# Optimization experiments

Hardware: AMD Instinct MI355X
Metric: run time of the kernel (lower is better)

The kernel has to match this reference:

```python
import jax, jax.numpy as jnp
import numpy as np

N_SPOTS = 50000
N_NEIGH = 32   # fixed-degree padding of the ragged radius-graph neighbor lists
N_PROG = 128


def setup_inputs() -> dict:
    key = jax.random.key(0)
    k1, k2, k3 = jax.random.split(key, 3)
    # soft identity probabilities (rows sum to 1, as in the original usage)
    probs = jax.random.uniform(k1, (N_SPOTS, N_PROG), dtype=jnp.float32)
    probs = probs / probs.sum(axis=-1, keepdims=True)
    # neighbor indices (fixed-degree representation of the ragged lists)
    neighbor_idx = jax.random.randint(k2, (N_SPOTS, N_NEIGH), 0, N_SPOTS)
    # gaussian-kernel weights, normalized per spot exactly as _build_graph does
    w = jax.random.uniform(k3, (N_SPOTS, N_NEIGH), dtype=jnp.float32) + 1e-6
    w = w / w.sum(axis=-1, keepdims=True)
    return {"identity_probs": probs, "weights": w, "neighbor_idx": neighbor_idx}


def reference(identity_probs, weights, neighbor_idx):
    # consistency_loss: (1/n) * sum_i sum_j w_ij * ||p_i - p_j||^2
    neigh = identity_probs[neighbor_idx]                 # [n, K, d] gather
    diff = identity_probs[:, None, :] - neigh            # [n, K, d]
    sq = jnp.sum(diff * diff, axis=-1)                   # [n, K]
    n = identity_probs.shape[0]
    return jnp.sum(weights * sq) / n
```

## Files before the change

### kernel.cpp

```cpp
#include <hip/hip_runtime.h>

#define N_SPOTS 50000
#define N_NEIGH 32
#define N_PROG  128

#define BLOCK 256
#define WPB   4

#define TAB_BYTES  ((size_t)N_SPOTS * 64)
#define PAIR_BYTES ((size_t)N_SPOTS * 8)

#define PREP_BLOCKS   3125
#define GATHER_BLOCKS 3125
#define F32_BLOCKS    6250

#if __has_builtin(__builtin_amdgcn_udot8)
__device__ __forceinline__ int dot8(unsigned a, unsigned b) {
    return __builtin_amdgcn_udot8(a, b, 0, false);
}
#else
__device__ __forceinline__ int dot8(unsigned a, unsigned b) {
    int s = 0;
    #pragma unroll
    for (int d = 0; d < 8; ++d)
        s += (int)((a >> (4 * d)) & 0xFu) * (int)((b >> (4 * d)) & 0xFu);
    return s;
}
#endif

__device__ __forceinline__ unsigned q4(float x, float r) {
    unsigned v = (unsigned)__builtin_fmaf(x, r, 0.5f);
    return v > 15u ? 15u : v;
}

__global__ __launch_bounds__(BLOCK) void prep_kernel(
    const float* __restrict__ probs,
    unsigned* __restrict__ tab,
    float2* __restrict__ pair)
{
    const int sub = threadIdx.x & 15;
    const int row = blockIdx.x * 16 + (threadIdx.x >> 4);

    const float* rp = probs + (size_t)row * N_PROG;
    const float4 a = *reinterpret_cast<const float4*>(rp + sub * 4);
    const float4 b = *reinterpret_cast<const float4*>(rp + 64 + sub * 4);

    float mx = fmaxf(fmaxf(a.x, a.y), fmaxf(a.z, a.w));
    mx = fmaxf(mx, fmaxf(fmaxf(b.x, b.y), fmaxf(b.z, b.w)));

    float nr = a.x * a.x;
    nr = fmaf(a.y, a.y, nr); nr = fmaf(a.z, a.z, nr); nr = fmaf(a.w, a.w, nr);
    nr = fmaf(b.x, b.x, nr); nr = fmaf(b.y, b.y, nr);
    nr = fmaf(b.z, b.z, nr); nr = fmaf(b.w, b.w, nr);

    #pragma unroll
    for (int off = 1; off < 16; off <<= 1) {
        mx  = fmaxf(mx, __shfl_xor(mx, off, 16));
        nr += __shfl_xor(nr, off, 16);
    }

    const float r = 15.0f / mx;
    unsigned q = q4(a.x, r);
    q |= q4(a.y, r) << 4;   q |= q4(a.z, r) << 8;   q |= q4(a.w, r) << 12;
    q |= q4(b.x, r) << 16;  q |= q4(b.y, r) << 20;
    q |= q4(b.z, r) << 24;  q |= q4(b.w, r) << 28;

    tab[row * 16 + sub] = q;
    if (sub == 0) pair[row] = make_float2(mx * (1.0f / 15.0f), nr);
}

__global__ __launch_bounds__(BLOCK) void gather_i4_kernel(
    const unsigned* __restrict__ tab,
    const float2* __restrict__ pair,
    const float* __restrict__ w,
    const int*   __restrict__ idx,
    float* __restrict__ partials)
{
    const int lane  = threadIdx.x & 63;
    const int sub   = lane & 15;
    const int wib   = threadIdx.x >> 6;
    const int grp16 = threadIdx.x >> 4;
    const int spot  = blockIdx.x * 16 + grp16;

    const unsigned pown = tab[spot * 16 + sub];
    const float2   pri  = pair[spot];
    const float    s_i  = pri.x, nrm_i = pri.y;

    const int   base = spot * N_NEIGH + sub;
    const int   i0 = idx[base], i1 = idx[base + 16];
    const float w0 = w[base],   w1 = w[base + 16];
    const float2 pr0 = pair[i0], pr1 = pair[i1];
    const float ws0 = w0 * s_i * pr0.x;
    const float ws1 = w1 * s_i * pr1.x;
    const float accB = fmaf(w0, pr0.y, w1 * pr1.y);
    const float accW = w0 + w1;

    __shared__ int2 stage[16][N_NEIGH];
    stage[grp16][sub]      = make_int2(i0, __float_as_int(ws0));
    stage[grp16][sub + 16] = make_int2(i1, __float_as_int(ws1));

    float accC = 0.0f;

    #pragma unroll
    for (int c = 0; c < 4; ++c) {
        unsigned q[8];
        float    wsj[8];
        #pragma unroll
        for (int k = 0; k < 8; ++k) {
            const int2 e = stage[grp16][c * 8 + k];
            wsj[k] = __int_as_float(e.y);
            q[k]   = tab[e.x * 16 + sub];
        }
        #pragma unroll
        for (int k = 0; k < 8; ++k) {
            accC = fmaf(wsj[k], (float)dot8(pown, q[k]), accC);
        }
    }

    float acc = fmaf(accW, nrm_i, accB) - 2.0f * accC;

    #pragma unroll
    for (int off = 32; off > 0; off >>= 1)
        acc += __shfl_down(acc, off, 64);

    __shared__ float s[WPB];
    if (lane == 0) s[wib] = acc;
    __syncthreads();
    if (threadIdx.x == 0) {
        float t = 0.0f;
        #pragma unroll
        for (int v = 0; v < WPB; ++v) t += s[v];
        partials[blockIdx.x] = t;
    }
}

__global__ __launch_bounds__(BLOCK) void gather_f32_kernel(
    const float* __restrict__ probs,
    const float* __restrict__ w,
    const int*   __restrict__ idx,
    float* __restrict__ partials)
{
    const int wib  = threadIdx.x >> 6;
    const int lane = threadIdx.x & 63;
    const int sub  = lane & 31;
    const int half = lane >> 5;
    const int wg   = blockIdx.x * WPB + wib;
    const int spot = (wg << 1) + half;

    const float4 p = *reinterpret_cast<const float4*>(
        probs + (size_t)spot * N_PROG + sub * 4);
    const int   my_idx = idx[spot * N_NEIGH + sub];
    const float my_w   = w  [spot * N_NEIGH + sub];

    float acc = 0.0f;
    #pragma unroll 8
    for (int j = 0; j < N_NEIGH; ++j) {
        const int   nb = __shfl(my_idx, j, 32);
        const float wj = __shfl(my_w,   j, 32);
        const float4 q = *reinterpret_cast<const float4*>(
            probs + (size_t)nb * N_PROG + sub * 4);
        const float dx = p.x - q.x, dy = p.y - q.y;
        const float dz = p.z - q.z, dw = p.w - q.w;
        float sq = dx * dx;
        sq = fmaf(dy, dy, sq); sq = fmaf(dz, dz, sq); sq = fmaf(dw, dw, sq);
        acc = fmaf(wj, sq, acc);
    }

    #pragma unroll
    for (int off = 32; off > 0; off >>= 1)
        acc += __shfl_down(acc, off, 64);

    __shared__ float s[WPB];
    if (lane == 0) s[wib] = acc;
    __syncthreads();
    if (threadIdx.x == 0) {
        float t = 0.0f;
        #pragma unroll
        for (int v = 0; v < WPB; ++v) t += s[v];
        partials[blockIdx.x] = t;
    }
}

__global__ __launch_bounds__(BLOCK) void finalize_kernel(
    const float* __restrict__ partials, int nparts, float* __restrict__ out)
{
    const int wave = threadIdx.x >> 6;
    const int lane = threadIdx.x & 63;

    float acc = 0.0f;
    for (int i = threadIdx.x; i < nparts; i += BLOCK)
        acc += partials[i];

    #pragma unroll
    for (int off = 32; off > 0; off >>= 1)
        acc += __shfl_down(acc, off, 64);

    __shared__ float s[WPB];
    if (lane == 0) s[wave] = acc;
    __syncthreads();
    if (threadIdx.x == 0) {
        float t = 0.0f;
        #pragma unroll
        for (int v = 0; v < WPB; ++v) t += s[v];
        out[0] = t / (float)N_SPOTS;
    }
}

extern "C" void kernel_launch(void* const* d_in, const int* in_sizes, int n_in,
                              void* d_out, int out_size, void* d_ws, size_t ws_size,
                              hipStream_t stream) {
    const float* probs = (const float*)d_in[0];
    const float* w     = (const float*)d_in[1];
    const int*   idx   = (const int*)  d_in[2];
    float* out = (float*)d_out;

    const size_t need = TAB_BYTES + PAIR_BYTES + GATHER_BLOCKS * sizeof(float);
    if (ws_size >= need) {
        unsigned* tab   = (unsigned*)d_ws;
        float2*   pair  = (float2*)((char*)d_ws + TAB_BYTES);
        float* partials = (float*)((char*)d_ws + TAB_BYTES + PAIR_BYTES);

        prep_kernel     <<<PREP_BLOCKS,   BLOCK, 0, stream>>>(probs, tab, pair);
        gather_i4_kernel<<<GATHER_BLOCKS, BLOCK, 0, stream>>>(tab, pair, w, idx, partials);
        finalize_kernel <<<1,             BLOCK, 0, stream>>>(partials, GATHER_BLOCKS, out);
    } else {
        float* partials = (float*)d_ws;
        gather_f32_kernel<<<F32_BLOCKS, BLOCK, 0, stream>>>(probs, w, idx, partials);
        finalize_kernel  <<<1,          BLOCK, 0, stream>>>(partials, F32_BLOCKS, out);
    }
}
```

Baseline: 34.21 us.

## Quantize with a global max scale and fuse the final reduction into the gather

```diff
diff --git a/kernel.cpp b/kernel.cpp
--- a/kernel.cpp
+++ b/kernel.cpp
@@ -7,12 +7,17 @@
 #define BLOCK 256
 #define WPB   4
 
-#define TAB_BYTES  ((size_t)N_SPOTS * 64)
-#define PAIR_BYTES ((size_t)N_SPOTS * 8)
-
-#define PREP_BLOCKS   3125
+#define MAX_BLOCKS    256
+#define QUANT_BLOCKS  3125
 #define GATHER_BLOCKS 3125
 #define F32_BLOCKS    6250
+
+#define TAB_BYTES  ((size_t)N_SPOTS * 64)
+#define BMAX_OFF   TAB_BYTES
+#define GSLOT_OFF  (BMAX_OFF + 1024)
+#define TICKET_OFF (GSLOT_OFF + 64)
+#define PART_OFF   (TICKET_OFF + 64)
+#define NEED_BYTES (PART_OFF + (size_t)GATHER_BLOCKS * 4)
 
 #if __has_builtin(__builtin_amdgcn_udot8)
 __device__ __forceinline__ int dot8(unsigned a, unsigned b) {
@@ -33,48 +38,64 @@
     return v > 15u ? 15u : v;
 }
 
-__global__ __launch_bounds__(BLOCK) void prep_kernel(
-    const float* __restrict__ probs,
-    unsigned* __restrict__ tab,
-    float2* __restrict__ pair)
-{
-    const int sub = threadIdx.x & 15;
-    const int row = blockIdx.x * 16 + (threadIdx.x >> 4);
-
-    const float* rp = probs + (size_t)row * N_PROG;
-    const float4 a = *reinterpret_cast<const float4*>(rp + sub * 4);
-    const float4 b = *reinterpret_cast<const float4*>(rp + 64 + sub * 4);
-
-    float mx = fmaxf(fmaxf(a.x, a.y), fmaxf(a.z, a.w));
-    mx = fmaxf(mx, fmaxf(fmaxf(b.x, b.y), fmaxf(b.z, b.w)));
-
-    float nr = a.x * a.x;
-    nr = fmaf(a.y, a.y, nr); nr = fmaf(a.z, a.z, nr); nr = fmaf(a.w, a.w, nr);
-    nr = fmaf(b.x, b.x, nr); nr = fmaf(b.y, b.y, nr);
-    nr = fmaf(b.z, b.z, nr); nr = fmaf(b.w, b.w, nr);
-
-    #pragma unroll
-    for (int off = 1; off < 16; off <<= 1) {
-        mx  = fmaxf(mx, __shfl_xor(mx, off, 16));
-        nr += __shfl_xor(nr, off, 16);
-    }
-
-    const float r = 15.0f / mx;
+__global__ __launch_bounds__(BLOCK) void max_kernel(
+    const float* __restrict__ probs, float* __restrict__ blockmax,
+    unsigned* __restrict__ ticket)
+{
+    const float4* p4 = reinterpret_cast<const float4*>(probs);
+    float m = 0.0f;
+    for (int i = blockIdx.x * BLOCK + threadIdx.x; i < (N_SPOTS * N_PROG / 4);
+         i += MAX_BLOCKS * BLOCK) {
+        const float4 v = p4[i];
+        m = fmaxf(m, fmaxf(fmaxf(v.x, v.y), fmaxf(v.z, v.w)));
+    }
+    #pragma unroll
+    for (int off = 32; off > 0; off >>= 1) m = fmaxf(m, __shfl_down(m, off, 64));
+    __shared__ float s[WPB];
+    if ((threadIdx.x & 63) == 0) s[threadIdx.x >> 6] = m;
+    __syncthreads();
+    if (threadIdx.x == 0) {
+        blockmax[blockIdx.x] = fmaxf(fmaxf(s[0], s[1]), fmaxf(s[2], s[3]));
+        if (blockIdx.x == 0) *ticket = 0u;
+    }
+}
+
+__global__ __launch_bounds__(BLOCK) void quant_kernel(
+    const float* __restrict__ probs, const float* __restrict__ blockmax,
+    unsigned* __restrict__ tab, float* __restrict__ gslot)
+{
+    __shared__ float smax[WPB];
+    __shared__ float gsh;
+    float m = blockmax[threadIdx.x];
+    #pragma unroll
+    for (int off = 32; off > 0; off >>= 1) m = fmaxf(m, __shfl_down(m, off, 64));
+    if ((threadIdx.x & 63) == 0) smax[threadIdx.x >> 6] = m;
+    __syncthreads();
+    if (threadIdx.x == 0)
+        gsh = fmaxf(fmaxf(smax[0], smax[1]), fmaxf(smax[2], smax[3]));
+    __syncthreads();
+    const float r = 15.0f / gsh;
+
+    const int t = blockIdx.x * BLOCK + threadIdx.x;
+    const float* rp = probs + (size_t)t * 8;
+    const float4 a = *reinterpret_cast<const float4*>(rp);
+    const float4 b = *reinterpret_cast<const float4*>(rp + 4);
     unsigned q = q4(a.x, r);
     q |= q4(a.y, r) << 4;   q |= q4(a.z, r) << 8;   q |= q4(a.w, r) << 12;
     q |= q4(b.x, r) << 16;  q |= q4(b.y, r) << 20;
     q |= q4(b.z, r) << 24;  q |= q4(b.w, r) << 28;
-
-    tab[row * 16 + sub] = q;
-    if (sub == 0) pair[row] = make_float2(mx * (1.0f / 15.0f), nr);
-}
-
-__global__ __launch_bounds__(BLOCK) void gather_i4_kernel(
+    tab[t] = q;
+    if (t == 0) gslot[0] = gsh;
+}
+
+__global__ __launch_bounds__(BLOCK) void gather_kernel(
     const unsigned* __restrict__ tab,
-    const float2* __restrict__ pair,
     const float* __restrict__ w,
     const int*   __restrict__ idx,
-    float* __restrict__ partials)
+    const float* __restrict__ gslot,
+    float* __restrict__ partials,
+    unsigned* __restrict__ ticket,
+    float* __restrict__ out)
 {
     const int lane  = threadIdx.x & 63;
     const int sub   = lane & 15;
@@ -83,54 +104,67 @@
     const int spot  = blockIdx.x * 16 + grp16;
 
     const unsigned pown = tab[spot * 16 + sub];
-    const float2   pri  = pair[spot];
-    const float    s_i  = pri.x, nrm_i = pri.y;
+    const int Qi2 = dot8(pown, pown);
 
     const int   base = spot * N_NEIGH + sub;
     const int   i0 = idx[base], i1 = idx[base + 16];
     const float w0 = w[base],   w1 = w[base + 16];
-    const float2 pr0 = pair[i0], pr1 = pair[i1];
-    const float ws0 = w0 * s_i * pr0.x;
-    const float ws1 = w1 * s_i * pr1.x;
-    const float accB = fmaf(w0, pr0.y, w1 * pr1.y);
-    const float accW = w0 + w1;
+
+    float sw = w0 + w1;
+    #pragma unroll
+    for (int off = 1; off < 16; off <<= 1) sw += __shfl_xor(sw, off, 16);
 
     __shared__ int2 stage[16][N_NEIGH];
-    stage[grp16][sub]      = make_int2(i0, __float_as_int(ws0));
-    stage[grp16][sub + 16] = make_int2(i1, __float_as_int(ws1));
-
-    float accC = 0.0f;
-
+    stage[grp16][sub]      = make_int2(i0, __float_as_int(w0));
+    stage[grp16][sub + 16] = make_int2(i1, __float_as_int(w1));
+
+    float acc2 = 0.0f;
     #pragma unroll
     for (int c = 0; c < 4; ++c) {
-        unsigned q[8];
-        float    wsj[8];
+        unsigned q[8]; float wj[8];
         #pragma unroll
         for (int k = 0; k < 8; ++k) {
             const int2 e = stage[grp16][c * 8 + k];
-            wsj[k] = __int_as_float(e.y);
-            q[k]   = tab[e.x * 16 + sub];
+            wj[k] = __int_as_float(e.y);
+            q[k]  = tab[e.x * 16 + sub];
         }
         #pragma unroll
         for (int k = 0; k < 8; ++k) {
-            accC = fmaf(wsj[k], (float)dot8(pown, q[k]), accC);
+            const int D  = dot8(pown, q[k]);
+            const int Q2 = dot8(q[k], q[k]);
+            acc2 = fmaf(wj[k], (float)(Q2 - 2 * D), acc2);
         }
     }
 
-    float acc = fmaf(accW, nrm_i, accB) - 2.0f * accC;
+    const float G    = gslot[0];
+    const float step = G * (1.0f / 15.0f);
+    float contrib = fmaf(sw, (float)Qi2 - (4.0f / 3.0f), acc2) * (step * step);
 
     #pragma unroll
     for (int off = 32; off > 0; off >>= 1)
-        acc += __shfl_down(acc, off, 64);
-
-    __shared__ float s[WPB];
-    if (lane == 0) s[wib] = acc;
-    __syncthreads();
-    if (threadIdx.x == 0) {
-        float t = 0.0f;
-        #pragma unroll
-        for (int v = 0; v < WPB; ++v) t += s[v];
-        partials[blockIdx.x] = t;
+        contrib += __shfl_down(contrib, off, 64);
+
+    __shared__ float sred[WPB];
+    __shared__ bool  slast;
+    if (lane == 0) sred[wib] = contrib;
+    __syncthreads();
+    if (threadIdx.x == 0) {
+        partials[blockIdx.x] = sred[0] + sred[1] + sred[2] + sred[3];
+        __threadfence();
+        const unsigned old = atomicAdd(ticket, 1u);
+        slast = (old == GATHER_BLOCKS - 1);
+    }
+    __syncthreads();
+    if (slast) {
+        __threadfence();
+        float a = 0.0f;
+        for (int i = threadIdx.x; i < GATHER_BLOCKS; i += BLOCK) a += partials[i];
+        #pragma unroll
+        for (int off = 32; off > 0; off >>= 1) a += __shfl_down(a, off, 64);
+        if (lane == 0) sred[wib] = a;
+        __syncthreads();
+        if (threadIdx.x == 0)
+            out[0] = (sred[0] + sred[1] + sred[2] + sred[3]) / (float)N_SPOTS;
     }
 }
 
@@ -165,11 +199,8 @@
         sq = fmaf(dy, dy, sq); sq = fmaf(dz, dz, sq); sq = fmaf(dw, dw, sq);
         acc = fmaf(wj, sq, acc);
     }
-
-    #pragma unroll
-    for (int off = 32; off > 0; off >>= 1)
-        acc += __shfl_down(acc, off, 64);
-
+    #pragma unroll
+    for (int off = 32; off > 0; off >>= 1) acc += __shfl_down(acc, off, 64);
     __shared__ float s[WPB];
     if (lane == 0) s[wib] = acc;
     __syncthreads();
@@ -186,15 +217,10 @@
 {
     const int wave = threadIdx.x >> 6;
     const int lane = threadIdx.x & 63;
-
     float acc = 0.0f;
-    for (int i = threadIdx.x; i < nparts; i += BLOCK)
-        acc += partials[i];
-
-    #pragma unroll
-    for (int off = 32; off > 0; off >>= 1)
-        acc += __shfl_down(acc, off, 64);
-
+    for (int i = threadIdx.x; i < nparts; i += BLOCK) acc += partials[i];
+    #pragma unroll
+    for (int off = 32; off > 0; off >>= 1) acc += __shfl_down(acc, off, 64);
     __shared__ float s[WPB];
     if (lane == 0) s[wave] = acc;
     __syncthreads();
@@ -214,15 +240,17 @@
     const int*   idx   = (const int*)  d_in[2];
     float* out = (float*)d_out;
 
-    const size_t need = TAB_BYTES + PAIR_BYTES + GATHER_BLOCKS * sizeof(float);
-    if (ws_size >= need) {
-        unsigned* tab   = (unsigned*)d_ws;
-        float2*   pair  = (float2*)((char*)d_ws + TAB_BYTES);
-        float* partials = (float*)((char*)d_ws + TAB_BYTES + PAIR_BYTES);
-
-        prep_kernel     <<<PREP_BLOCKS,   BLOCK, 0, stream>>>(probs, tab, pair);
-        gather_i4_kernel<<<GATHER_BLOCKS, BLOCK, 0, stream>>>(tab, pair, w, idx, partials);
-        finalize_kernel <<<1,             BLOCK, 0, stream>>>(partials, GATHER_BLOCKS, out);
+    if (ws_size >= NEED_BYTES) {
+        unsigned* tab      = (unsigned*)d_ws;
+        float*    blockmax = (float*)((char*)d_ws + BMAX_OFF);
+        float*    gslot    = (float*)((char*)d_ws + GSLOT_OFF);
+        unsigned* ticket   = (unsigned*)((char*)d_ws + TICKET_OFF);
+        float*    partials = (float*)((char*)d_ws + PART_OFF);
+
+        max_kernel   <<<MAX_BLOCKS,    BLOCK, 0, stream>>>(probs, blockmax, ticket);
+        quant_kernel <<<QUANT_BLOCKS,  BLOCK, 0, stream>>>(probs, blockmax, tab, gslot);
+        gather_kernel<<<GATHER_BLOCKS, BLOCK, 0, stream>>>(tab, w, idx, gslot,
+                                                           partials, ticket, out);
     } else {
         float* partials = (float*)d_ws;
         gather_f32_kernel<<<F32_BLOCKS, BLOCK, 0, stream>>>(probs, w, idx, partials);
```

New measurement: 97.89 us. +186.2%, slower.
